# Kernel optimization log

Hardware: AMD Instinct MI355X
Metric: run time of the kernel (lower is better)

Reference implementation:

```python
import jax, jax.numpy as jnp
import numpy as np

NUM_ENTITIES = 100000
NUM_RELATIONS = 8
NUM_CLASSES = 16
HIDDEN = 16
NUM_EDGES = 3200000


def rgcn_conv(x, src, dst, edge_type, W, root, bias):
    """PyG-style RGCNConv: out_i = x_i @ root + bias + sum_r mean_{j in N_r(i)} x_j @ W_r."""
    num_nodes = x.shape[0]
    x_src = x[src]  # [E, d_in] gather
    # per-edge message x_j @ W_{edge_type}: accumulate over the small fixed relation set
    msg = jnp.zeros((src.shape[0], W.shape[2]), x.dtype)
    for r in range(NUM_RELATIONS):
        msg = msg + jnp.where((edge_type == r)[:, None], x_src @ W[r], jnp.zeros((), x.dtype))
    # per-(dst, relation) edge counts for mean aggregation
    cnt = jnp.zeros((num_nodes, NUM_RELATIONS), x.dtype).at[dst, edge_type].add(1.0)
    norm = 1.0 / jnp.maximum(cnt[dst, edge_type], 1.0)  # [E]
    agg = jax.ops.segment_sum(msg * norm[:, None], dst, num_segments=num_nodes)
    return agg + x @ root + bias


def setup_inputs() -> dict:
    key = jax.random.key(0)
    ks = jax.random.split(key, 9)
    s = 1.0 / np.sqrt(HIDDEN)
    edge_index = jax.random.randint(ks[0], (2, NUM_EDGES), 0, NUM_ENTITIES, dtype=jnp.int32)
    edge_type = jax.random.randint(ks[1], (NUM_EDGES,), 0, NUM_RELATIONS, dtype=jnp.int32)
    return {
        "embed": jax.random.normal(ks[2], (NUM_ENTITIES, HIDDEN), jnp.float32),
        "W1": jax.random.normal(ks[3], (NUM_RELATIONS, HIDDEN, HIDDEN), jnp.float32) * s,
        "root1": jax.random.normal(ks[4], (HIDDEN, HIDDEN), jnp.float32) * s,
        "b1": jnp.zeros((HIDDEN,), jnp.float32),
        "W2": jax.random.normal(ks[5], (NUM_RELATIONS, HIDDEN, NUM_CLASSES), jnp.float32) * s,
        "root2": jax.random.normal(ks[6], (HIDDEN, NUM_CLASSES), jnp.float32) * s,
        "b2": jnp.zeros((NUM_CLASSES,), jnp.float32),
        "edge_index": edge_index,
        "edge_type": edge_type,
    }


def reference(embed, W1, root1, b1, W2, root2, b2, edge_index, edge_type):
    src, dst = edge_index[0], edge_index[1]
    h = rgcn_conv(embed, src, dst, edge_type, W1, root1, b1)
    h = jax.nn.relu(h)
    h = rgcn_conv(h, src, dst, edge_type, W2, root2, b2)
    return jax.nn.log_softmax(h, axis=1)
```

## Files before the change

### kernel.cpp

```cpp
#include <hip/hip_runtime.h>


constexpr int NN = 100000;
constexpr int NE = 3200000;
constexpr int NFINE = 1563;
constexpr int NCOARSE = 49;
constexpr int CAP = 3072;
constexpr int SST = 136;

typedef short bf16x8 __attribute__((ext_vector_type(8)));
typedef float f32x4 __attribute__((ext_vector_type(4)));

__device__ __forceinline__ short f2bf(float f) {
  union { float f; unsigned u; } v; v.f = f;
  unsigned r = v.u + 0x7FFFu + ((v.u >> 16) & 1u);
  return (short)(r >> 16);
}

__global__ void __launch_bounds__(256) conv_kernel(
    const float* __restrict__ X, unsigned short* __restrict__ Xb) {
  int i = blockIdx.x * 256 + threadIdx.x;
  if (i < NN * 4) {
    float4 v = reinterpret_cast<const float4*>(X)[i];
    ushort4 o;
    o.x = (unsigned short)f2bf(v.x); o.y = (unsigned short)f2bf(v.y);
    o.z = (unsigned short)f2bf(v.z); o.w = (unsigned short)f2bf(v.w);
    reinterpret_cast<ushort4*>(Xb)[i] = o;
  }
}

__global__ void __launch_bounds__(256) hist_kernel(
    const int* __restrict__ dst, unsigned* __restrict__ fcnt) {
  __shared__ unsigned h[NFINE];
  for (int i = threadIdx.x; i < NFINE; i += 256) h[i] = 0u;
  __syncthreads();
  const int base = blockIdx.x * 8192;
#pragma unroll
  for (int i = 0; i < 32; ++i) {
    int e = base + i * 256 + threadIdx.x;
    if (e < NE) atomicAdd(&h[(unsigned)dst[e] >> 6], 1u);
  }
  __syncthreads();
  for (int i = threadIdx.x; i < NFINE; i += 256)
    if (h[i]) atomicAdd(&fcnt[i], h[i]);
}

__global__ void __launch_bounds__(256) scan_kernel(
    const unsigned* __restrict__ fcnt, unsigned* __restrict__ foff,
    unsigned* __restrict__ fcur, unsigned* __restrict__ cbnd,
    unsigned* __restrict__ ccur) {
  __shared__ unsigned sh[256];
  unsigned v[7], s = 0;
#pragma unroll
  for (int j = 0; j < 7; ++j) {
    int idx = threadIdx.x * 7 + j;
    v[j] = (idx < NFINE) ? fcnt[idx] : 0u;
    s += v[j];
  }
  sh[threadIdx.x] = s;
  __syncthreads();
  for (int d = 1; d < 256; d <<= 1) {
    unsigned t = (threadIdx.x >= d) ? sh[threadIdx.x - d] : 0u;
    __syncthreads();
    sh[threadIdx.x] += t;
    __syncthreads();
  }
  unsigned run = sh[threadIdx.x] - s;
#pragma unroll
  for (int j = 0; j < 7; ++j) {
    int idx = threadIdx.x * 7 + j;
    if (idx <= NFINE) foff[idx] = run;
    if (idx < NFINE) fcur[idx] = run;
    run += v[j];
  }
  __syncthreads();
  if (threadIdx.x <= NCOARSE) {
    int f = threadIdx.x * 32; if (f > NFINE) f = NFINE;
    unsigned b = foff[f];
    cbnd[threadIdx.x] = b;
    if (threadIdx.x < NCOARSE) ccur[threadIdx.x] = b;
  }
}

__global__ void __launch_bounds__(256) part1_kernel(
    const int* __restrict__ src, const int* __restrict__ dst,
    const int* __restrict__ typ, unsigned* __restrict__ ccur,
    unsigned* __restrict__ buf1) {
  __shared__ unsigned hist[NCOARSE];
  __shared__ unsigned gb[NCOARSE];
  if (threadIdx.x < NCOARSE) hist[threadIdx.x] = 0u;
  __syncthreads();
  const int base = blockIdx.x * 4096;
  unsigned ent[16], cb[16], rk[16];
#pragma unroll
  for (int i = 0; i < 16; ++i) {
    int e = base + i * 256 + threadIdx.x;
    if (e < NE) {
      unsigned d = (unsigned)dst[e];
      ent[i] = (unsigned)src[e] | ((unsigned)typ[e] << 17) | ((d & 2047u) << 20);
      cb[i] = d >> 11;
      rk[i] = atomicAdd(&hist[cb[i]], 1u);
    } else cb[i] = 0xFFFFFFFFu;
  }
  __syncthreads();
  if (threadIdx.x < NCOARSE && hist[threadIdx.x])
    gb[threadIdx.x] = atomicAdd(&ccur[threadIdx.x], hist[threadIdx.x]);
  __syncthreads();
#pragma unroll
  for (int i = 0; i < 16; ++i)
    if (cb[i] != 0xFFFFFFFFu) buf1[gb[cb[i]] + rk[i]] = ent[i];
}

__global__ void __launch_bounds__(256) part2_kernel(
    const unsigned* __restrict__ buf1, const unsigned* __restrict__ cbnd,
    unsigned* __restrict__ fcur, unsigned* __restrict__ buf2) {
  __shared__ unsigned hist[NFINE];
  __shared__ unsigned gb[NFINE];
  __shared__ unsigned cb_s[NCOARSE + 1];
  for (int i = threadIdx.x; i < NFINE; i += 256) hist[i] = 0u;
  if (threadIdx.x <= NCOARSE) cb_s[threadIdx.x] = cbnd[threadIdx.x];
  __syncthreads();
  const unsigned base = blockIdx.x * 4096u;
  int cc = 0;
  while (cc < NCOARSE - 1 && base >= cb_s[cc + 1]) ++cc;
  unsigned ent[16], fn[16], rk[16];
#pragma unroll
  for (int i = 0; i < 16; ++i) {
    unsigned p = base + i * 256u + threadIdx.x;
    if (p < (unsigned)NE) {
      unsigned e = buf1[p];
      while (p >= cb_s[cc + 1]) ++cc;
      fn[i] = (unsigned)cc * 32u + ((e >> 26) & 31u);
      ent[i] = e & 0x03FFFFFFu;
      rk[i] = atomicAdd(&hist[fn[i]], 1u);
    } else fn[i] = 0xFFFFFFFFu;
  }
  __syncthreads();
  for (int i = threadIdx.x; i < NFINE; i += 256)
    if (hist[i]) gb[i] = atomicAdd(&fcur[i], hist[i]);
  __syncthreads();
#pragma unroll
  for (int i = 0; i < 16; ++i)
    if (fn[i] != 0xFFFFFFFFu) buf2[gb[fn[i]] + rk[i]] = ent[i];
}

template <int MODE>
__global__ void __launch_bounds__(512) layer_kernel(
    const unsigned short* __restrict__ Xb, const float* __restrict__ W,
    const float* __restrict__ ROOT, const float* __restrict__ BIAS,
    const unsigned* __restrict__ foff, const unsigned* __restrict__ buf2,
    unsigned short* __restrict__ Hout, float* __restrict__ Fout) {
  __shared__ unsigned short S[64 * SST];
  __shared__ unsigned E[CAP];
  __shared__ unsigned cnt512[512];
  __shared__ unsigned cur512[512];
  __shared__ unsigned wsum[8];
  const int tid = threadIdx.x;

  cnt512[tid] = 0u;
#pragma unroll
  for (int i = 0; i < CAP / 512; ++i) E[tid + i * 512] = 0u;
  __syncthreads();

  const unsigned p0 = foff[blockIdx.x];
  const int seg = (int)(foff[blockIdx.x + 1] - p0);

  unsigned e_0 = 0xFFFFFFFFu, e_1 = 0xFFFFFFFFu, e_2 = 0xFFFFFFFFu,
           e_3 = 0xFFFFFFFFu, e_4 = 0xFFFFFFFFu, e_5 = 0xFFFFFFFFu;
  if (tid < seg)          e_0 = buf2[p0 + tid];
  if (tid + 512 < seg)    e_1 = buf2[p0 + tid + 512];
  if (tid + 1024 < seg)   e_2 = buf2[p0 + tid + 1024];
  if (tid + 1536 < seg)   e_3 = buf2[p0 + tid + 1536];
  if (tid + 2048 < seg)   e_4 = buf2[p0 + tid + 2048];
  if (tid + 2560 < seg)   e_5 = buf2[p0 + tid + 2560];
  auto BIN = [](unsigned e) -> unsigned { return (e >> 17) & 511u; };
  auto HB = [&](unsigned e) {
    if (e != 0xFFFFFFFFu) atomicAdd(&cnt512[BIN(e)], 1u);
  };
  HB(e_0); HB(e_1); HB(e_2); HB(e_3); HB(e_4); HB(e_5);
  __syncthreads();

  unsigned own = cnt512[tid];
  unsigned incl = own;
#pragma unroll
  for (int d = 1; d < 64; d <<= 1) {
    unsigned t = __shfl_up(incl, d, 64);
    if ((tid & 63) >= d) incl += t;
  }
  if ((tid & 63) == 63) wsum[tid >> 6] = incl;
  __syncthreads();
  unsigned pre = 0;
#pragma unroll
  for (int wv = 0; wv < 8; ++wv)
    pre += (wv < (tid >> 6)) ? wsum[wv] : 0u;
  cur512[tid] = pre + incl - own;
  __syncthreads();

  auto SC = [&](unsigned e) {
    if (e != 0xFFFFFFFFu) {
      unsigned pos = atomicAdd(&cur512[BIN(e)], 1u);
      if (pos < (unsigned)CAP) E[pos] = e;
    }
  };
  SC(e_0); SC(e_1); SC(e_2); SC(e_3); SC(e_4); SC(e_5);
  __syncthreads();

  const int w = tid >> 6;
  const int lane = tid & 63;
  const int rc = lane & 15;
  const int quad = lane >> 4;

  for (int pq = 0; pq < 4; ++pq) {
    const int pp = w * 4 + pq;
    const int pb = pp * 16;
    const int beg = (int)(cur512[pb] - cnt512[pb]);
    const int end = (int)cur512[pb + 15];
    const unsigned rowbin = (unsigned)(pb + rc);

    f32x4 acc = {0.f, 0.f, 0.f, 0.f};
    int p = beg;
    for (; p + 32 <= end; p += 32) {
      bf16x8 af, bv;
#pragma unroll
      for (int j = 0; j < 8; ++j) {
        unsigned e = E[p + quad * 8 + j];
        af[j] = (((e >> 17) & 511u) == rowbin) ? (short)0x3F80 : (short)0;
        bv[j] = (short)Xb[(size_t)(e & 0x1FFFFu) * 16 + rc];
      }
      acc = __builtin_amdgcn_mfma_f32_16x16x32_bf16(af, bv, acc, 0, 0, 0);
    }
    if (p < end) {
      bf16x8 af, bv;
#pragma unroll
      for (int j = 0; j < 8; ++j) {
        int q = p + quad * 8 + j;
        unsigned e = E[q < CAP ? q : 0];
        bool v = q < end;
        af[j] = (v && ((e >> 17) & 511u) == rowbin) ? (short)0x3F80 : (short)0;
        bv[j] = (short)Xb[(size_t)(e & 0x1FFFFu) * 16 + rc];
      }
      acc = __builtin_amdgcn_mfma_f32_16x16x32_bf16(af, bv, acc, 0, 0, 0);
    }

#pragma unroll
    for (int r2 = 0; r2 < 4; ++r2) {
      int gbin = pb + quad * 4 + r2;
      unsigned ct = cnt512[gbin];
      float iv = 1.f / (float)(ct ? ct : 1u);
      int nd = gbin >> 3, rl = gbin & 7;
      S[nd * SST + rl * 16 + rc] = (unsigned short)f2bf(acc[r2] * iv);
    }
  }
  __syncthreads();

  if (w >= 4) return;
  const int fc = lane & 15;
  const int g = lane >> 4;
  const int n0 = blockIdx.x * 64 + w * 16;

  bf16x8 b0, b1, b2, b3, brt;
#pragma unroll
  for (int j = 0; j < 8; ++j) {
    int kq = g * 8 + j; int rb = kq >> 4; int kk = kq & 15;
    b0[j] = f2bf(W[(rb + 0) * 256 + kk * 16 + fc]);
    b1[j] = f2bf(W[(rb + 2) * 256 + kk * 16 + fc]);
    b2[j] = f2bf(W[(rb + 4) * 256 + kk * 16 + fc]);
    b3[j] = f2bf(W[(rb + 6) * 256 + kk * 16 + fc]);
    brt[j] = (kq < 16) ? f2bf(ROOT[kq * 16 + fc]) : (short)0;
  }

  const int kk0 = (g & 1) * 8;
  const int rsel = g >> 1;
  const int dl16 = w * 16 + fc;
  bf16x8 a0, a1, a2, a3;
#define LDA(AM, M)                                                        \
  {                                                                       \
    const unsigned short* sp2 = S + dl16 * SST + (2 * (M) + rsel) * 16 + kk0; \
    AM = *reinterpret_cast<const bf16x8*>(sp2);                           \
  }
  LDA(a0, 0) LDA(a1, 1) LDA(a2, 2) LDA(a3, 3)
#undef LDA

  bf16x8 ar = {0, 0, 0, 0, 0, 0, 0, 0};
  if (g < 2) {
    int node = n0 + fc;
    if (node < NN)
      ar = *reinterpret_cast<const bf16x8*>(Xb + (size_t)node * 16 + g * 8);
  }

  const float bc = BIAS[fc];
  f32x4 acc = {bc, bc, bc, bc};
  acc = __builtin_amdgcn_mfma_f32_16x16x32_bf16(a0, b0, acc, 0, 0, 0);
  acc = __builtin_amdgcn_mfma_f32_16x16x32_bf16(a1, b1, acc, 0, 0, 0);
  acc = __builtin_amdgcn_mfma_f32_16x16x32_bf16(a2, b2, acc, 0, 0, 0);
  acc = __builtin_amdgcn_mfma_f32_16x16x32_bf16(a3, b3, acc, 0, 0, 0);
  acc = __builtin_amdgcn_mfma_f32_16x16x32_bf16(ar, brt, acc, 0, 0, 0);

  if (MODE == 0) {
#pragma unroll
    for (int r2 = 0; r2 < 4; ++r2) {
      int node = n0 + g * 4 + r2;
      if (node < NN)
        Hout[(size_t)node * 16 + fc] = (unsigned short)f2bf(fmaxf(acc[r2], 0.f));
    }
  } else {
#pragma unroll
    for (int r2 = 0; r2 < 4; ++r2) {
      int node = n0 + g * 4 + r2;
      float zv = acc[r2];
      float mx = zv;
      mx = fmaxf(mx, __shfl_xor(mx, 1));
      mx = fmaxf(mx, __shfl_xor(mx, 2));
      mx = fmaxf(mx, __shfl_xor(mx, 4));
      mx = fmaxf(mx, __shfl_xor(mx, 8));
      float sm = expf(zv - mx);
      sm += __shfl_xor(sm, 1);
      sm += __shfl_xor(sm, 2);
      sm += __shfl_xor(sm, 4);
      sm += __shfl_xor(sm, 8);
      if (node < NN)
        Fout[(size_t)node * 16 + fc] = zv - mx - logf(sm);
    }
  }
}

extern "C" void kernel_launch(void* const* d_in, const int* in_sizes, int n_in,
                              void* d_out, int out_size, void* d_ws, size_t ws_size,
                              hipStream_t stream) {
  const float* embed = (const float*)d_in[0];
  const float* W1    = (const float*)d_in[1];
  const float* root1 = (const float*)d_in[2];
  const float* b1    = (const float*)d_in[3];
  const float* W2    = (const float*)d_in[4];
  const float* root2 = (const float*)d_in[5];
  const float* b2    = (const float*)d_in[6];
  const int* eidx    = (const int*)d_in[7];
  const int* etyp    = (const int*)d_in[8];
  const int* src = eidx;
  const int* dst = eidx + NE;
  float* out = (float*)d_out;

  unsigned* fcnt = (unsigned*)d_ws;
  unsigned* foff = fcnt + 1600;
  unsigned* fcur = foff + 1600;
  unsigned* cbnd = fcur + 1600;
  unsigned* ccur = cbnd + 64;
  unsigned* buf1 = ccur + 64;
  unsigned* buf2 = buf1 + NE;
  unsigned short* h  = (unsigned short*)buf1;
  unsigned short* xb = (unsigned short*)(buf1 + 800000);

  hipMemsetAsync(fcnt, 0, 1600 * 4, stream);
  hist_kernel<<<391, 256, 0, stream>>>(dst, fcnt);
  scan_kernel<<<1, 256, 0, stream>>>(fcnt, foff, fcur, cbnd, ccur);
  part1_kernel<<<782, 256, 0, stream>>>(src, dst, etyp, ccur, buf1);
  part2_kernel<<<782, 256, 0, stream>>>(buf1, cbnd, fcur, buf2);
  conv_kernel<<<1563, 256, 0, stream>>>(embed, xb);
  layer_kernel<0><<<NFINE, 512, 0, stream>>>(xb, W1, root1, b1, foff,
                                             buf2, h, out);
  layer_kernel<1><<<NFINE, 512, 0, stream>>>(h, W2, root2, b2, foff,
                                             buf2, h, out);
}
```

Baseline: 241.6 us.

## Restructure two-level edge partition with per-coarse-bucket fine histograms

The single fine-grained histogram over dst is replaced by a coarse 49-bucket histogram with a wave-shuffle scan. After the first partition pass, a new kernel builds the fine histogram by reading each coarse bucket's slice of buf1, followed by a separate fine scan. part2 now runs one block per (coarse bucket, slice) with only 32 shared counters instead of 1563-entry shared histograms, which cuts shared-memory init and contention. In exchange it adds two kernel launches and an extra read of buf1, and part2's per-element shared atomic ordering is no longer deterministic within a slice.

```diff
diff --git a/kernel.cpp b/kernel.cpp
--- a/kernel.cpp
+++ b/kernel.cpp
@@ -5,6 +5,7 @@
 constexpr int NE = 3200000;
 constexpr int NFINE = 1563;
 constexpr int NCOARSE = 49;
+constexpr int NSLICE = 16;
 constexpr int CAP = 3072;
 constexpr int SST = 136;
 
@@ -29,57 +30,36 @@
   }
 }
 
-__global__ void __launch_bounds__(256) hist_kernel(
-    const int* __restrict__ dst, unsigned* __restrict__ fcnt) {
-  __shared__ unsigned h[NFINE];
-  for (int i = threadIdx.x; i < NFINE; i += 256) h[i] = 0u;
+__global__ void __launch_bounds__(256) chist_kernel(
+    const int* __restrict__ dst, unsigned* __restrict__ ccnt) {
+  __shared__ unsigned h[NCOARSE];
+  if (threadIdx.x < NCOARSE) h[threadIdx.x] = 0u;
   __syncthreads();
   const int base = blockIdx.x * 8192;
 #pragma unroll
   for (int i = 0; i < 32; ++i) {
     int e = base + i * 256 + threadIdx.x;
-    if (e < NE) atomicAdd(&h[(unsigned)dst[e] >> 6], 1u);
-  }
-  __syncthreads();
-  for (int i = threadIdx.x; i < NFINE; i += 256)
-    if (h[i]) atomicAdd(&fcnt[i], h[i]);
-}
-
-__global__ void __launch_bounds__(256) scan_kernel(
-    const unsigned* __restrict__ fcnt, unsigned* __restrict__ foff,
-    unsigned* __restrict__ fcur, unsigned* __restrict__ cbnd,
+    if (e < NE) atomicAdd(&h[(unsigned)dst[e] >> 11], 1u);
+  }
+  __syncthreads();
+  if (threadIdx.x < NCOARSE && h[threadIdx.x])
+    atomicAdd(&ccnt[threadIdx.x], h[threadIdx.x]);
+}
+
+__global__ void __launch_bounds__(64) cscan_kernel(
+    const unsigned* __restrict__ ccnt, unsigned* __restrict__ cbnd,
     unsigned* __restrict__ ccur) {
-  __shared__ unsigned sh[256];
-  unsigned v[7], s = 0;
-#pragma unroll
-  for (int j = 0; j < 7; ++j) {
-    int idx = threadIdx.x * 7 + j;
-    v[j] = (idx < NFINE) ? fcnt[idx] : 0u;
-    s += v[j];
-  }
-  sh[threadIdx.x] = s;
-  __syncthreads();
-  for (int d = 1; d < 256; d <<= 1) {
-    unsigned t = (threadIdx.x >= d) ? sh[threadIdx.x - d] : 0u;
-    __syncthreads();
-    sh[threadIdx.x] += t;
-    __syncthreads();
-  }
-  unsigned run = sh[threadIdx.x] - s;
-#pragma unroll
-  for (int j = 0; j < 7; ++j) {
-    int idx = threadIdx.x * 7 + j;
-    if (idx <= NFINE) foff[idx] = run;
-    if (idx < NFINE) fcur[idx] = run;
-    run += v[j];
-  }
-  __syncthreads();
-  if (threadIdx.x <= NCOARSE) {
-    int f = threadIdx.x * 32; if (f > NFINE) f = NFINE;
-    unsigned b = foff[f];
-    cbnd[threadIdx.x] = b;
-    if (threadIdx.x < NCOARSE) ccur[threadIdx.x] = b;
-  }
+  int t = threadIdx.x;
+  unsigned v = (t < NCOARSE) ? ccnt[t] : 0u;
+  unsigned incl = v;
+#pragma unroll
+  for (int d = 1; d < 64; d <<= 1) {
+    unsigned u = __shfl_up(incl, d, 64);
+    if (t >= d) incl += u;
+  }
+  unsigned excl = incl - v;
+  if (t <= NCOARSE) cbnd[t] = excl;
+  if (t < NCOARSE) ccur[t] = excl;
 }
 
 __global__ void __launch_bounds__(256) part1_kernel(
@@ -111,37 +91,78 @@
     if (cb[i] != 0xFFFFFFFFu) buf1[gb[cb[i]] + rk[i]] = ent[i];
 }
 
+__global__ void __launch_bounds__(256) fhist_kernel(
+    const unsigned* __restrict__ buf1, const unsigned* __restrict__ cbnd,
+    unsigned* __restrict__ fcnt) {
+  __shared__ unsigned h[32];
+  const int c = blockIdx.x / NSLICE, s = blockIdx.x % NSLICE;
+  const unsigned b0 = cbnd[c], b1 = cbnd[c + 1];
+  const unsigned len = b1 - b0, sl = (len + NSLICE - 1) / NSLICE;
+  const unsigned lo = b0 + s * sl;
+  const unsigned hi = (lo + sl < b1) ? (lo + sl) : b1;
+  if (threadIdx.x < 32) h[threadIdx.x] = 0u;
+  __syncthreads();
+  for (unsigned p = lo + threadIdx.x; p < hi; p += 256)
+    atomicAdd(&h[(buf1[p] >> 26) & 31u], 1u);
+  __syncthreads();
+  if (threadIdx.x < 32 && h[threadIdx.x])
+    atomicAdd(&fcnt[c * 32 + threadIdx.x], h[threadIdx.x]);
+}
+
+__global__ void __launch_bounds__(256) fscan_kernel(
+    const unsigned* __restrict__ fcnt, unsigned* __restrict__ foff,
+    unsigned* __restrict__ fcur) {
+  __shared__ unsigned sh[256];
+  unsigned v[7], s = 0;
+#pragma unroll
+  for (int j = 0; j < 7; ++j) {
+    int idx = threadIdx.x * 7 + j;
+    v[j] = (idx < NFINE) ? fcnt[idx] : 0u;
+    s += v[j];
+  }
+  sh[threadIdx.x] = s;
+  __syncthreads();
+  for (int d = 1; d < 256; d <<= 1) {
+    unsigned t = (threadIdx.x >= d) ? sh[threadIdx.x - d] : 0u;
+    __syncthreads();
+    sh[threadIdx.x] += t;
+    __syncthreads();
+  }
+  unsigned run = sh[threadIdx.x] - s;
+#pragma unroll
+  for (int j = 0; j < 7; ++j) {
+    int idx = threadIdx.x * 7 + j;
+    if (idx <= NFINE) foff[idx] = run;
+    if (idx < NFINE) fcur[idx] = run;
+    run += v[j];
+  }
+}
+
 __global__ void __launch_bounds__(256) part2_kernel(
     const unsigned* __restrict__ buf1, const unsigned* __restrict__ cbnd,
     unsigned* __restrict__ fcur, unsigned* __restrict__ buf2) {
-  __shared__ unsigned hist[NFINE];
-  __shared__ unsigned gb[NFINE];
-  __shared__ unsigned cb_s[NCOARSE + 1];
-  for (int i = threadIdx.x; i < NFINE; i += 256) hist[i] = 0u;
-  if (threadIdx.x <= NCOARSE) cb_s[threadIdx.x] = cbnd[threadIdx.x];
-  __syncthreads();
-  const unsigned base = blockIdx.x * 4096u;
-  int cc = 0;
-  while (cc < NCOARSE - 1 && base >= cb_s[cc + 1]) ++cc;
-  unsigned ent[16], fn[16], rk[16];
-#pragma unroll
-  for (int i = 0; i < 16; ++i) {
-    unsigned p = base + i * 256u + threadIdx.x;
-    if (p < (unsigned)NE) {
-      unsigned e = buf1[p];
-      while (p >= cb_s[cc + 1]) ++cc;
-      fn[i] = (unsigned)cc * 32u + ((e >> 26) & 31u);
-      ent[i] = e & 0x03FFFFFFu;
-      rk[i] = atomicAdd(&hist[fn[i]], 1u);
-    } else fn[i] = 0xFFFFFFFFu;
-  }
-  __syncthreads();
-  for (int i = threadIdx.x; i < NFINE; i += 256)
-    if (hist[i]) gb[i] = atomicAdd(&fcur[i], hist[i]);
-  __syncthreads();
-#pragma unroll
-  for (int i = 0; i < 16; ++i)
-    if (fn[i] != 0xFFFFFFFFu) buf2[gb[fn[i]] + rk[i]] = ent[i];
+  __shared__ unsigned h[32], gb[32], cur[32];
+  const int c = blockIdx.x / NSLICE, s = blockIdx.x % NSLICE;
+  const unsigned b0 = cbnd[c], b1 = cbnd[c + 1];
+  const unsigned len = b1 - b0, sl = (len + NSLICE - 1) / NSLICE;
+  const unsigned lo = b0 + s * sl;
+  const unsigned hi = (lo + sl < b1) ? (lo + sl) : b1;
+  if (threadIdx.x < 32) { h[threadIdx.x] = 0u; cur[threadIdx.x] = 0u; }
+  __syncthreads();
+  for (unsigned p = lo + threadIdx.x; p < hi; p += 256)
+    atomicAdd(&h[(buf1[p] >> 26) & 31u], 1u);
+  __syncthreads();
+  if (threadIdx.x < 32) {
+    unsigned n = h[threadIdx.x];
+    gb[threadIdx.x] = n ? atomicAdd(&fcur[c * 32 + threadIdx.x], n) : 0u;
+  }
+  __syncthreads();
+  for (unsigned p = lo + threadIdx.x; p < hi; p += 256) {
+    unsigned e = buf1[p];
+    unsigned fl = (e >> 26) & 31u;
+    unsigned pos = gb[fl] + atomicAdd(&cur[fl], 1u);
+    buf2[pos] = e & 0x03FFFFFFu;
+  }
 }
 
 template <int MODE>
@@ -341,7 +362,8 @@
   float* out = (float*)d_out;
 
   unsigned* fcnt = (unsigned*)d_ws;
-  unsigned* foff = fcnt + 1600;
+  unsigned* ccnt = fcnt + 1600;
+  unsigned* foff = ccnt + 64;
   unsigned* fcur = foff + 1600;
   unsigned* cbnd = fcur + 1600;
   unsigned* ccur = cbnd + 64;
@@ -350,11 +372,13 @@
   unsigned short* h  = (unsigned short*)buf1;
   unsigned short* xb = (unsigned short*)(buf1 + 800000);
 
-  hipMemsetAsync(fcnt, 0, 1600 * 4, stream);
-  hist_kernel<<<391, 256, 0, stream>>>(dst, fcnt);
-  scan_kernel<<<1, 256, 0, stream>>>(fcnt, foff, fcur, cbnd, ccur);
+  hipMemsetAsync(fcnt, 0, (1600 + 64) * 4, stream);
+  chist_kernel<<<391, 256, 0, stream>>>(dst, ccnt);
+  cscan_kernel<<<1, 64, 0, stream>>>(ccnt, cbnd, ccur);
   part1_kernel<<<782, 256, 0, stream>>>(src, dst, etyp, ccur, buf1);
-  part2_kernel<<<782, 256, 0, stream>>>(buf1, cbnd, fcur, buf2);
+  fhist_kernel<<<NCOARSE * NSLICE, 256, 0, stream>>>(buf1, cbnd, fcnt);
+  fscan_kernel<<<1, 256, 0, stream>>>(fcnt, foff, fcur);
+  part2_kernel<<<NCOARSE * NSLICE, 256, 0, stream>>>(buf1, cbnd, fcur, buf2);
   conv_kernel<<<1563, 256, 0, stream>>>(embed, xb);
   layer_kernel<0><<<NFINE, 512, 0, stream>>>(xb, W1, root1, b1, foff,
                                              buf2, h, out);
```

Result: no change. 246.3 us (+1.9%).
